# Optimization experiments

Hardware: AMD Instinct MI355X
Metric: run time of the kernel (lower is better)

## Reference

```python
import jax, jax.numpy as jnp
import numpy as np

D_MODEL = 1024
HEADS = 16
D_K = D_MODEL // HEADS
B, S = 2, 2048
NEG = -1e9


def setup_inputs() -> dict:
    key = jax.random.key(0)
    ks = jax.random.split(key, 12)
    sc = 1.0 / np.sqrt(D_MODEL)
    inp = {
        'query': jax.random.normal(ks[0], (B, S, D_MODEL), jnp.float32),
        'key': jax.random.normal(ks[1], (B, S, D_MODEL), jnp.float32),
        'value': jax.random.normal(ks[2], (B, S, D_MODEL), jnp.float32),
        'mask': jnp.tril(jnp.ones((S, S), jnp.int32))[None, None],  # [1,1,S,S] causal
        'Wq': jax.random.normal(ks[3], (D_MODEL, D_MODEL), jnp.float32) * sc,
        'bq': jax.random.normal(ks[4], (D_MODEL,), jnp.float32) * 0.02,
        'Wk': jax.random.normal(ks[5], (D_MODEL, D_MODEL), jnp.float32) * sc,
        'bk': jax.random.normal(ks[6], (D_MODEL,), jnp.float32) * 0.02,
        'Wv': jax.random.normal(ks[7], (D_MODEL, D_MODEL), jnp.float32) * sc,
        'bv': jax.random.normal(ks[8], (D_MODEL,), jnp.float32) * 0.02,
        'Wo': jax.random.normal(ks[9], (D_MODEL, D_MODEL), jnp.float32) * sc,
        'bo': jax.random.normal(ks[10], (D_MODEL,), jnp.float32) * 0.02,
    }
    return inp


def reference(query, key, value, mask, Wq, bq, Wk, bk, Wv, bv, Wo, bo):
    # QKV projections (torch Linear: x @ W.T + b; here W stored as [in,out])
    def split_heads(x):  # [B,S,D] -> [B,H,S,dk]
        return x.reshape(B, S, HEADS, D_K).transpose(0, 2, 1, 3)

    q = split_heads(query @ Wq + bq)
    k = split_heads(key @ Wk + bk)
    v = split_heads(value @ Wv + bv)

    scores = jnp.einsum('bhqd,bhkd->bhqk', q, k) / np.sqrt(D_K)
    scores = jnp.where(mask == 0, NEG, scores)
    attn = jax.nn.softmax(scores, axis=-1)  # dropout p=0 (eval) -> identity
    out = jnp.einsum('bhqk,bhkd->bhqd', attn, v)
    out = out.transpose(0, 2, 1, 3).reshape(B, S, D_MODEL)
    return out @ Wo + bo
```

## Files before the change

### kernel.cpp

```cpp
#include <hip/hip_runtime.h>
#include <hip/hip_bf16.h>
#include <cstdint>
#include <cstddef>

typedef short short8 __attribute__((ext_vector_type(8)));
typedef float f32x4 __attribute__((ext_vector_type(4)));

#define SS 2048
#define DK 64
#define LAMBDA 0.18033688011112042f

__device__ __forceinline__ float b2f(ushort u) {
    union { uint32_t i; float f; } x; x.i = ((uint32_t)u) << 16; return x.f;
}
__device__ __forceinline__ ushort f2b(float f) {
    union { float f; uint32_t i; } x; x.f = f;
    uint32_t r = (x.i + 0x7fffu + ((x.i >> 16) & 1u)) >> 16;
    return (ushort)r;
}
__device__ __forceinline__ uint32_t pk_bf16(float a, float b) {
    union { __hip_bfloat162 v; uint32_t u; } x;
    float2 f2; f2.x = a; f2.y = b;
    x.v = __float22bfloat162_rn(f2);
    return x.u;
}

__device__ __forceinline__ void gl_lds16(const ushort* __restrict__ g, ushort* l) {
    __builtin_amdgcn_global_load_lds(
        (const __attribute__((address_space(1))) uint32_t*)(uintptr_t)g,
        (__attribute__((address_space(3))) uint32_t*)(uintptr_t)l, 16, 0, 0);
}

__device__ __forceinline__ bool probe_bf16(const uint32_t* __restrict__ probe) {
    const int lane = threadIdx.x & 63;
    int c = 0;
#pragma unroll
    for (int i = 0; i < 4; ++i) {
        uint32_t u = probe[lane * 4 + i];
        uint32_t e = (u >> 7) & 0xffu;
        c += (e >= 100u && e <= 140u) ? 1 : 0;
    }
    unsigned long long b = __ballot(c >= 3);
    return __popcll(b) > 32;
}

__device__ __forceinline__ void ld8_f32_to_bf16(ushort* dst, const float* __restrict__ src) {
    float4 a = *(const float4*)src;
    float4 b = *(const float4*)(src + 4);
    ushort t[8] = {f2b(a.x), f2b(a.y), f2b(a.z), f2b(a.w),
                   f2b(b.x), f2b(b.y), f2b(b.z), f2b(b.w)};
    *(uint4*)dst = *(uint4*)t;
}

__global__ __launch_bounds__(256) void transpose_all(const void* __restrict__ W0,
                                                     const void* __restrict__ W1,
                                                     const void* __restrict__ W2,
                                                     const void* __restrict__ W3,
                                                     ushort* __restrict__ ws,
                                                     const uint32_t* __restrict__ probe,
                                                     size_t wotOff) {
    __shared__ __align__(16) ushort t[64 * 72];
    const bool isbf = probe_bf16(probe);
    const int z = blockIdx.z;
    const void* W = (z == 0) ? W0 : (z == 1) ? W1 : (z == 2) ? W2 : W3;
    ushort* T = ws + ((z < 3) ? ((size_t)z << 20) : wotOff);

    const int n0 = blockIdx.x * 64, k0 = blockIdx.y * 64;
    const int tid = threadIdx.x;
    const int r = tid >> 3, cg = (tid & 7) * 8;
    if (isbf) {
        const ushort* Wb = (const ushort*)W;
#pragma unroll
        for (int p = 0; p < 2; ++p) {
            int k = r + p * 32;
            *(uint4*)&t[k * 72 + cg] = *(const uint4*)&Wb[(size_t)(k0 + k) * 1024 + n0 + cg];
        }
    } else {
        const float* Wf = (const float*)W;
#pragma unroll
        for (int p = 0; p < 2; ++p) {
            int k = r + p * 32;
            ld8_f32_to_bf16(&t[k * 72 + cg], &Wf[(size_t)(k0 + k) * 1024 + n0 + cg]);
        }
    }
    __syncthreads();
#pragma unroll
    for (int p = 0; p < 2; ++p) {
        int n = r + p * 32;
        uint4 o;
        ushort* op = (ushort*)&o;
#pragma unroll
        for (int i = 0; i < 8; ++i) op[i] = t[(cg + i) * 72 + n];
        *(uint4*)&T[(size_t)(n0 + n) * 1024 + k0 + cg] = o;
    }
}

__global__ __launch_bounds__(256) void conv_qkv(const void* __restrict__ q,
                                                const void* __restrict__ k,
                                                const void* __restrict__ v,
                                                ushort* __restrict__ ws,
                                                const uint32_t* __restrict__ probe,
                                                size_t dstOff) {
    const bool isbf = probe_bf16(probe);
    const int z = blockIdx.y;
    const void* src = (z == 0) ? q : (z == 1) ? k : v;
    ushort* dst = ws + dstOff + ((size_t)z << 22);
    const size_t i = ((size_t)blockIdx.x * 256 + threadIdx.x) * 8;
    if (isbf)
        *(uint4*)&dst[i] = *(const uint4*)&((const ushort*)src)[i];
    else
        ld8_f32_to_bf16(&dst[i], &((const float*)src)[i]);
}

template <int PRE>
__global__ __launch_bounds__(256) void qkv_gemm(const void* __restrict__ qp,
                                                const void* __restrict__ kp,
                                                const void* __restrict__ vp,
                                                const void* __restrict__ bqp,
                                                const void* __restrict__ bkp,
                                                const void* __restrict__ bvp,
                                                ushort* __restrict__ ws,
                                                const uint32_t* __restrict__ probe) {
    __shared__ __align__(16) ushort As[128 * 32];
    __shared__ __align__(16) ushort Bs[128 * 32];
    const bool isbf = probe_bf16(probe);
    const int z = blockIdx.z;
    const ushort* Bt = ws + ((size_t)z << 20);
    const void* bias = (z == 0) ? bqp : (z == 1) ? bkp : bvp;
    ushort* C = ws + ((size_t)((PRE ? 16 : 5) + 4 * z) << 20);
    const float scl = (z == 0) ? LAMBDA : 1.0f;

    const int tid = threadIdx.x;
    const int lane = tid & 63, wid = tid >> 6;
    const int l15 = lane & 15, g = lane >> 4;
    const int wm = wid >> 1, wn = wid & 1;
    const int m0 = blockIdx.y * 128, n0 = blockIdx.x * 128;
    const int sr = tid >> 2, sc = (tid & 3) * 8;
    const int lrow = (lane >> 2), lcol = (lane & 3) * 8;

    f32x4 acc[4][4];
#pragma unroll
    for (int i = 0; i < 4; ++i)
#pragma unroll
        for (int j = 0; j < 4; ++j) {
            f32x4 zz = {0.f, 0.f, 0.f, 0.f};
            acc[i][j] = zz;
        }

    for (int kk = 0; kk < 1024; kk += 32) {
        __syncthreads();
#pragma unroll
        for (int q = 0; q < 2; ++q) {
            const int row = (wid * 2 + q) * 16 + lrow;
            gl_lds16(&Bt[(size_t)(n0 + row) * 1024 + kk + lcol], &Bs[(wid * 2 + q) * 512]);
        }
        if (PRE) {
            const ushort* Ab = ws + ((size_t)(4 + 4 * z) << 20);
#pragma unroll
            for (int q = 0; q < 2; ++q) {
                const int row = (wid * 2 + q) * 16 + lrow;
                gl_lds16(&Ab[(size_t)(m0 + row) * 1024 + kk + lcol], &As[(wid * 2 + q) * 512]);
            }
        } else {
            const void* A = (z == 0) ? qp : (z == 1) ? kp : vp;
            if (isbf) {
                const ushort* Ab = (const ushort*)A;
#pragma unroll
                for (int q = 0; q < 2; ++q) {
                    const int row = (wid * 2 + q) * 16 + lrow;
                    gl_lds16(&Ab[(size_t)(m0 + row) * 1024 + kk + lcol], &As[(wid * 2 + q) * 512]);
                }
            } else {
                const float* Af = (const float*)A;
                ld8_f32_to_bf16(&As[sr * 32 + sc], &Af[(size_t)(m0 + sr) * 1024 + kk + sc]);
                ld8_f32_to_bf16(&As[(sr + 64) * 32 + sc],
                                &Af[(size_t)(m0 + sr + 64) * 1024 + kk + sc]);
            }
        }
        __syncthreads();
        short8 a[4], b[4];
#pragma unroll
        for (int i = 0; i < 4; ++i) a[i] = *(const short8*)&As[(wm * 64 + i * 16 + l15) * 32 + g * 8];
#pragma unroll
        for (int j = 0; j < 4; ++j) b[j] = *(const short8*)&Bs[(wn * 64 + j * 16 + l15) * 32 + g * 8];
#pragma unroll
        for (int i = 0; i < 4; ++i)
#pragma unroll
            for (int j = 0; j < 4; ++j)
                acc[i][j] = __builtin_amdgcn_mfma_f32_16x16x32_bf16(a[i], b[j], acc[i][j], 0, 0, 0);
    }

#pragma unroll
    for (int i = 0; i < 4; ++i)
#pragma unroll
        for (int j = 0; j < 4; ++j) {
            const int col = n0 + wn * 64 + j * 16 + l15;
            const float bv = isbf ? b2f(((const ushort*)bias)[col]) : ((const float*)bias)[col];
#pragma unroll
            for (int r = 0; r < 4; ++r) {
                const int row = m0 + wm * 64 + i * 16 + g * 4 + r;
                const float v = (acc[i][j][r] + bv) * scl;
                size_t idx;
                if (z != 2) {
                    idx = ((size_t)((row >> 11) * 16 + (col >> 6)) * SS + (row & 2047)) * 64 +
                          (col & 63);
                } else {
                    idx = ((size_t)((row >> 11) * 16 + (col >> 6)) * 64 + (col & 63)) * SS +
                          (row & 2047);
                }
                C[idx] = f2b(v);
            }
        }
}

__global__ __launch_bounds__(256) void out_gemm(const ushort* __restrict__ A,
                                                const ushort* __restrict__ Bt,
                                                const void* __restrict__ bias,
                                                void* __restrict__ C,
                                                const uint32_t* __restrict__ probe) {
    __shared__ __align__(16) ushort As[64 * 32];
    __shared__ __align__(16) ushort Bs[128 * 32];
    const bool isbf = probe_bf16(probe);
    const int tid = threadIdx.x;
    const int lane = tid & 63, wid = tid >> 6;
    const int l15 = lane & 15, g = lane >> 4;
    const int wm = wid >> 1, wn = wid & 1;
    const int m0 = blockIdx.y * 64, n0 = blockIdx.x * 128;
    const int lrow = (lane >> 2), lcol = (lane & 3) * 8;

    f32x4 acc[2][4];
#pragma unroll
    for (int i = 0; i < 2; ++i)
#pragma unroll
        for (int j = 0; j < 4; ++j) {
            f32x4 zz = {0.f, 0.f, 0.f, 0.f};
            acc[i][j] = zz;
        }

    for (int kk = 0; kk < 1024; kk += 32) {
        __syncthreads();
        {
            const int row = wid * 16 + lrow;
            gl_lds16(&A[(size_t)(m0 + row) * 1024 + kk + lcol], &As[wid * 512]);
        }
#pragma unroll
        for (int q = 0; q < 2; ++q) {
            const int row = (wid * 2 + q) * 16 + lrow;
            gl_lds16(&Bt[(size_t)(n0 + row) * 1024 + kk + lcol], &Bs[(wid * 2 + q) * 512]);
        }
        __syncthreads();
        short8 a[2], b[4];
#pragma unroll
        for (int i = 0; i < 2; ++i) a[i] = *(const short8*)&As[(wm * 32 + i * 16 + l15) * 32 + g * 8];
#pragma unroll
        for (int j = 0; j < 4; ++j) b[j] = *(const short8*)&Bs[(wn * 64 + j * 16 + l15) * 32 + g * 8];
#pragma unroll
        for (int i = 0; i < 2; ++i)
#pragma unroll
            for (int j = 0; j < 4; ++j)
                acc[i][j] = __builtin_amdgcn_mfma_f32_16x16x32_bf16(a[i], b[j], acc[i][j], 0, 0, 0);
    }

#pragma unroll
    for (int i = 0; i < 2; ++i)
#pragma unroll
        for (int j = 0; j < 4; ++j) {
            const int col = n0 + wn * 64 + j * 16 + l15;
            const float bv = isbf ? b2f(((const ushort*)bias)[col]) : ((const float*)bias)[col];
#pragma unroll
            for (int r = 0; r < 4; ++r) {
                const int row = m0 + wm * 32 + i * 16 + g * 4 + r;
                const float v = acc[i][j][r] + bv;
                const size_t idx = (size_t)row * 1024 + col;
                if (isbf)
                    ((ushort*)C)[idx] = f2b(v);
                else
                    ((float*)C)[idx] = v;
            }
        }
}

__global__ __launch_bounds__(256, 3) void attn_fwd(const ushort* __restrict__ Q,
                                                   const ushort* __restrict__ K,
                                                   const ushort* __restrict__ Vt,
                                                   ushort* __restrict__ O) {
    __shared__ __align__(16) ushort Ks[2][64 * 64];
    __shared__ __align__(16) ushort Vs[2][64 * 64];
    __shared__ __align__(16) ushort Ps[4][32 * 64];

    const int y = blockIdx.y;
    const int s0i = (blockIdx.x + y) & 15;
    const int t = (y & 16) ? (15 - s0i) : s0i;
    const int tid = threadIdx.x;
    const int lane = tid & 63, wid = tid >> 6;
    const int l15 = lane & 15, g = lane >> 4;
    const int sw = l15 & 7;

    const ushort* Qb = Q + (size_t)y * SS * DK;
    const ushort* Kb = K + (size_t)y * SS * DK;
    const ushort* Vb = Vt + (size_t)y * DK * SS;
    const int b = y >> 4, h = y & 15;

    const int q0 = t * 128 + wid * 32;
    const int nkt = 2 * t + 2;

    const int srow = lane >> 3;
    const int sgc = ((lane & 7) ^ srow) * 8;
    ushort* Pw = Ps[wid];

    short8 qf[2][2];
#pragma unroll
    for (int mt = 0; mt < 2; ++mt)
#pragma unroll
        for (int c = 0; c < 2; ++c)
            qf[mt][c] =
                *(const short8*)&Qb[(size_t)(q0 + mt * 16 + l15) * 64 + c * 32 + g * 8];

    f32x4 acc_o[2][4];
#pragma unroll
    for (int mt = 0; mt < 2; ++mt)
#pragma unroll
        for (int jt = 0; jt < 4; ++jt) {
            f32x4 zz = {0.f, 0.f, 0.f, 0.f};
            acc_o[mt][jt] = zz;
        }
    float lp[2][4];
#pragma unroll
    for (int mt = 0; mt < 2; ++mt)
#pragma unroll
        for (int r = 0; r < 4; ++r) lp[mt][r] = 0.f;

#pragma unroll
    for (int i = 0; i < 2; ++i) {
        const int chunk = wid * 2 + i;
        const int row = chunk * 8 + srow;
        gl_lds16(&Kb[(size_t)row * 64 + sgc], &Ks[0][chunk * 512]);
        gl_lds16(&Vb[(size_t)row * SS + sgc], &Vs[0][chunk * 512]);
    }
    __syncthreads();

#pragma unroll 1
    for (int kt = 0; kt < nkt; ++kt) {
        const int cur = kt & 1;
        if (kt + 1 < nkt) {
            const int k0n = (kt + 1) * 64;
#pragma unroll
            for (int i = 0; i < 2; ++i) {
                const int chunk = wid * 2 + i;
                const int row = chunk * 8 + srow;
                gl_lds16(&Kb[(size_t)(k0n + row) * 64 + sgc], &Ks[cur ^ 1][chunk * 512]);
                gl_lds16(&Vb[(size_t)row * SS + k0n + sgc], &Vs[cur ^ 1][chunk * 512]);
            }
        }

        f32x4 sc[2][4];
#pragma unroll
        for (int mt = 0; mt < 2; ++mt)
#pragma unroll
            for (int nt = 0; nt < 4; ++nt) {
                f32x4 zz = {0.f, 0.f, 0.f, 0.f};
                sc[mt][nt] = zz;
            }
#pragma unroll
        for (int c = 0; c < 2; ++c)
#pragma unroll
            for (int nt = 0; nt < 4; ++nt) {
                short8 kb =
                    *(const short8*)&Ks[cur][(nt * 16 + l15) * 64 + (((c * 4 + g) ^ sw) * 8)];
#pragma unroll
                for (int mt = 0; mt < 2; ++mt)
                    sc[mt][nt] =
                        __builtin_amdgcn_mfma_f32_16x16x32_bf16(qf[mt][c], kb, sc[mt][nt], 0, 0, 0);
            }

        if (kt >= nkt - 2) {
            const int k0 = kt * 64;
#pragma unroll
            for (int mt = 0; mt < 2; ++mt) {
                const int rowg = q0 + mt * 16 + g * 4;
#pragma unroll
                for (int nt = 0; nt < 4; ++nt) {
                    const int colg = k0 + nt * 16 + l15;
#pragma unroll
                    for (int r = 0; r < 4; ++r)
                        if (colg > rowg + r) sc[mt][nt][r] = -1e9f;
                }
            }
        }

#pragma unroll
        for (int mt = 0; mt < 2; ++mt)
#pragma unroll
            for (int r = 0; r < 4; ++r) {
                float ss = 0.f;
#pragma unroll
                for (int nt = 0; nt < 4; ++nt) {
                    const float p = exp2f(sc[mt][nt][r]);
                    sc[mt][nt][r] = p;
                    ss += p;
                }
                lp[mt][r] += ss;
            }

#pragma unroll
        for (int mt = 0; mt < 2; ++mt)
#pragma unroll
            for (int r = 0; r < 4; ++r) {
                const int pr = mt * 16 + g * 4 + r;
                const int prsw = (pr & 7);
                const int h8 = l15 >> 3, lo3 = l15 & 7;
#pragma unroll
                for (int pp = 0; pp < 2; ++pp) {
                    const uint32_t u = pk_bf16(sc[mt][2 * pp][r], sc[mt][2 * pp + 1][r]);
                    Pw[pr * 64 + (((2 * pp) * 2 + h8) ^ prsw) * 8 + lo3] = (ushort)(u & 0xffffu);
                    Pw[pr * 64 + (((2 * pp + 1) * 2 + h8) ^ prsw) * 8 + lo3] = (ushort)(u >> 16);
                }
            }

#pragma unroll
        for (int c2 = 0; c2 < 2; ++c2) {
            short8 pa[2];
#pragma unroll
            for (int mt = 0; mt < 2; ++mt)
                pa[mt] = *(const short8*)&Pw[(mt * 16 + l15) * 64 + (((c2 * 4 + g) ^ sw) * 8)];
#pragma unroll
            for (int jt = 0; jt < 4; ++jt) {
                short8 vb =
                    *(const short8*)&Vs[cur][(jt * 16 + l15) * 64 + (((c2 * 4 + g) ^ sw) * 8)];
#pragma unroll
                for (int mt = 0; mt < 2; ++mt)
                    acc_o[mt][jt] =
                        __builtin_amdgcn_mfma_f32_16x16x32_bf16(pa[mt], vb, acc_o[mt][jt], 0, 0, 0);
            }
        }

        __syncthreads();
    }

    float inv[2][4];
#pragma unroll
    for (int mt = 0; mt < 2; ++mt)
#pragma unroll
        for (int r = 0; r < 4; ++r) {
            float ss = lp[mt][r];
            ss += __shfl_xor(ss, 1);
            ss += __shfl_xor(ss, 2);
            ss += __shfl_xor(ss, 4);
            ss += __shfl_xor(ss, 8);
            inv[mt][r] = 1.0f / ss;
        }
#pragma unroll
    for (int mt = 0; mt < 2; ++mt)
#pragma unroll
        for (int jt = 0; jt < 4; ++jt)
#pragma unroll
            for (int r = 0; r < 4; ++r) {
                const int row = q0 + mt * 16 + g * 4 + r;
                const int col = h * 64 + jt * 16 + l15;
                O[(size_t)(b * SS + row) * 1024 + col] = f2b(acc_o[mt][jt][r] * inv[mt][r]);
            }
}

extern "C" void kernel_launch(void* const* d_in, const int* in_sizes, int n_in,
                              void* d_out, int out_size, void* d_ws, size_t ws_size,
                              hipStream_t stream) {
    const void* q = d_in[0];
    const void* k = d_in[1];
    const void* v = d_in[2];
    const void* Wq = d_in[4];
    const void* bq = d_in[5];
    const void* Wk = d_in[6];
    const void* bk = d_in[7];
    const void* Wv = d_in[8];
    const void* bv = d_in[9];
    const void* Wo = d_in[10];
    const void* bo = d_in[11];
    const uint32_t* probe = (const uint32_t*)d_in[0];

    ushort* ws = (ushort*)d_ws;
    const size_t M = (size_t)1 << 20;
    const bool pre = ws_size >= 28 * M * sizeof(ushort);

    if (pre) {
        transpose_all<<<dim3(16, 16, 4), 256, 0, stream>>>(Wq, Wk, Wv, Wo, ws, probe, 3 * M);
        conv_qkv<<<dim3(2048, 3), 256, 0, stream>>>(q, k, v, ws, probe, 4 * M);
        qkv_gemm<1><<<dim3(8, 32, 3), 256, 0, stream>>>(q, k, v, bq, bk, bv, ws, probe);
        attn_fwd<<<dim3(16, 32), 256, 0, stream>>>(ws + 16 * M, ws + 20 * M, ws + 24 * M,
                                                   ws + 4 * M);
        out_gemm<<<dim3(8, 64), 256, 0, stream>>>(ws + 4 * M, ws + 3 * M, bo, d_out, probe);
    } else {
        transpose_all<<<dim3(16, 16, 4), 256, 0, stream>>>(Wq, Wk, Wv, Wo, ws, probe, 4 * M);
        qkv_gemm<0><<<dim3(8, 32, 3), 256, 0, stream>>>(q, k, v, bq, bk, bv, ws, probe);
        attn_fwd<<<dim3(16, 32), 256, 0, stream>>>(ws + 5 * M, ws + 9 * M, ws + 13 * M, ws);
        out_gemm<<<dim3(8, 64), 256, 0, stream>>>(ws, ws + 4 * M, bo, d_out, probe);
    }
}
```

Baseline: 242.8 us.

## Rewrite attention inner loop with 32x32 MFMA and register-resident P via permlane swap

```diff
diff --git a/kernel.cpp b/kernel.cpp
--- a/kernel.cpp
+++ b/kernel.cpp
@@ -5,6 +5,7 @@
 
 typedef short short8 __attribute__((ext_vector_type(8)));
 typedef float f32x4 __attribute__((ext_vector_type(4)));
+typedef float f32x16 __attribute__((ext_vector_type(16)));
 
 #define SS 2048
 #define DK 64
@@ -280,55 +281,49 @@
         }
 }
 
-__global__ __launch_bounds__(256, 3) void attn_fwd(const ushort* __restrict__ Q,
+__global__ __launch_bounds__(256, 2) void attn_fwd(const ushort* __restrict__ Q,
                                                    const ushort* __restrict__ K,
                                                    const ushort* __restrict__ Vt,
                                                    ushort* __restrict__ O) {
     __shared__ __align__(16) ushort Ks[2][64 * 64];
     __shared__ __align__(16) ushort Vs[2][64 * 64];
-    __shared__ __align__(16) ushort Ps[4][32 * 64];
 
     const int y = blockIdx.y;
     const int s0i = (blockIdx.x + y) & 15;
     const int t = (y & 16) ? (15 - s0i) : s0i;
     const int tid = threadIdx.x;
     const int lane = tid & 63, wid = tid >> 6;
-    const int l15 = lane & 15, g = lane >> 4;
-    const int sw = l15 & 7;
+    const int l31 = lane & 31, h = lane >> 5;
 
     const ushort* Qb = Q + (size_t)y * SS * DK;
     const ushort* Kb = K + (size_t)y * SS * DK;
     const ushort* Vb = Vt + (size_t)y * DK * SS;
-    const int b = y >> 4, h = y & 15;
-
-    const int q0 = t * 128 + wid * 32;
+    const int b = y >> 4, hh = y & 15;
+
+    const int q0w = t * 128 + wid * 32;
     const int nkt = 2 * t + 2;
 
     const int srow = lane >> 3;
     const int sgc = ((lane & 7) ^ srow) * 8;
-    ushort* Pw = Ps[wid];
-
-    short8 qf[2][2];
-#pragma unroll
-    for (int mt = 0; mt < 2; ++mt)
-#pragma unroll
-        for (int c = 0; c < 2; ++c)
-            qf[mt][c] =
-                *(const short8*)&Qb[(size_t)(q0 + mt * 16 + l15) * 64 + c * 32 + g * 8];
-
-    f32x4 acc_o[2][4];
-#pragma unroll
-    for (int mt = 0; mt < 2; ++mt)
-#pragma unroll
-        for (int jt = 0; jt < 4; ++jt) {
-            f32x4 zz = {0.f, 0.f, 0.f, 0.f};
-            acc_o[mt][jt] = zz;
-        }
-    float lp[2][4];
-#pragma unroll
-    for (int mt = 0; mt < 2; ++mt)
-#pragma unroll
-        for (int r = 0; r < 4; ++r) lp[mt][r] = 0.f;
+
+    short8 qf[4];
+#pragma unroll
+    for (int k4 = 0; k4 < 4; ++k4)
+        qf[k4] = *(const short8*)&Qb[(size_t)(q0w + l31) * 64 + k4 * 16 + h * 8];
+
+    int foff[2][4];
+#pragma unroll
+    for (int aa = 0; aa < 2; ++aa)
+#pragma unroll
+        for (int k4 = 0; k4 < 4; ++k4)
+            foff[aa][k4] = (aa * 32 + l31) * 64 + (((k4 * 2 + h) ^ (l31 & 7)) * 8);
+
+    f32x16 acc[2];
+#pragma unroll
+    for (int nt = 0; nt < 2; ++nt)
+#pragma unroll
+        for (int r = 0; r < 16; ++r) acc[nt][r] = 0.f;
+    float lpA = 0.f, lpB = 0.f;
 
 #pragma unroll
     for (int i = 0; i < 2; ++i) {
@@ -353,112 +348,84 @@
             }
         }
 
-        f32x4 sc[2][4];
-#pragma unroll
-        for (int mt = 0; mt < 2; ++mt)
-#pragma unroll
-            for (int nt = 0; nt < 4; ++nt) {
-                f32x4 zz = {0.f, 0.f, 0.f, 0.f};
-                sc[mt][nt] = zz;
-            }
-#pragma unroll
-        for (int c = 0; c < 2; ++c)
-#pragma unroll
-            for (int nt = 0; nt < 4; ++nt) {
-                short8 kb =
-                    *(const short8*)&Ks[cur][(nt * 16 + l15) * 64 + (((c * 4 + g) ^ sw) * 8)];
-#pragma unroll
-                for (int mt = 0; mt < 2; ++mt)
-                    sc[mt][nt] =
-                        __builtin_amdgcn_mfma_f32_16x16x32_bf16(qf[mt][c], kb, sc[mt][nt], 0, 0, 0);
-            }
-
-        if (kt >= nkt - 2) {
-            const int k0 = kt * 64;
-#pragma unroll
-            for (int mt = 0; mt < 2; ++mt) {
-                const int rowg = q0 + mt * 16 + g * 4;
-#pragma unroll
-                for (int nt = 0; nt < 4; ++nt) {
-                    const int colg = k0 + nt * 16 + l15;
-#pragma unroll
-                    for (int r = 0; r < 4; ++r)
-                        if (colg > rowg + r) sc[mt][nt][r] = -1e9f;
+        if (q0w + 31 >= kt * 64) {
+            f32x16 sc[2];
+#pragma unroll
+            for (int st = 0; st < 2; ++st)
+#pragma unroll
+                for (int r = 0; r < 16; ++r) sc[st][r] = 0.f;
+#pragma unroll
+            for (int st = 0; st < 2; ++st)
+#pragma unroll
+                for (int k4 = 0; k4 < 4; ++k4) {
+                    short8 kb = *(const short8*)&Ks[cur][foff[st][k4]];
+                    sc[st] = __builtin_amdgcn_mfma_f32_32x32x16_bf16(kb, qf[k4], sc[st], 0, 0, 0);
                 }
-            }
-        }
-
-#pragma unroll
-        for (int mt = 0; mt < 2; ++mt)
-#pragma unroll
-            for (int r = 0; r < 4; ++r) {
-                float ss = 0.f;
-#pragma unroll
-                for (int nt = 0; nt < 4; ++nt) {
-                    const float p = exp2f(sc[mt][nt][r]);
-                    sc[mt][nt][r] = p;
-                    ss += p;
+
+            if (kt >= nkt - 2) {
+                const int qg = q0w + l31;
+#pragma unroll
+                for (int st = 0; st < 2; ++st)
+#pragma unroll
+                    for (int r = 0; r < 16; ++r) {
+                        const int kvg = kt * 64 + st * 32 + (r & 3) + 8 * (r >> 2) + 4 * h;
+                        if (kvg > qg) sc[st][r] = -1e9f;
+                    }
+            }
+
+            uint32_t pk8[2][8];
+#pragma unroll
+            for (int st = 0; st < 2; ++st) {
+                float ls = 0.f;
+#pragma unroll
+                for (int i = 0; i < 8; ++i) {
+                    const float p0 = exp2f(sc[st][2 * i]);
+                    const float p1 = exp2f(sc[st][2 * i + 1]);
+                    ls += p0 + p1;
+                    pk8[st][i] = pk_bf16(p0, p1);
                 }
-                lp[mt][r] += ss;
-            }
-
-#pragma unroll
-        for (int mt = 0; mt < 2; ++mt)
-#pragma unroll
-            for (int r = 0; r < 4; ++r) {
-                const int pr = mt * 16 + g * 4 + r;
-                const int prsw = (pr & 7);
-                const int h8 = l15 >> 3, lo3 = l15 & 7;
-#pragma unroll
-                for (int pp = 0; pp < 2; ++pp) {
-                    const uint32_t u = pk_bf16(sc[mt][2 * pp][r], sc[mt][2 * pp + 1][r]);
-                    Pw[pr * 64 + (((2 * pp) * 2 + h8) ^ prsw) * 8 + lo3] = (ushort)(u & 0xffffu);
-                    Pw[pr * 64 + (((2 * pp + 1) * 2 + h8) ^ prsw) * 8 + lo3] = (ushort)(u >> 16);
+                if (st == 0) lpA += ls; else lpB += ls;
+            }
+
+#pragma unroll
+            for (int st = 0; st < 2; ++st) {
+                asm("v_permlane32_swap_b32 %0, %1" : "+v"(pk8[st][0]), "+v"(pk8[st][2]));
+                asm("v_permlane32_swap_b32 %0, %1" : "+v"(pk8[st][1]), "+v"(pk8[st][3]));
+                asm("v_permlane32_swap_b32 %0, %1" : "+v"(pk8[st][4]), "+v"(pk8[st][6]));
+                asm("v_permlane32_swap_b32 %0, %1" : "+v"(pk8[st][5]), "+v"(pk8[st][7]));
+            }
+
+#pragma unroll
+            for (int ktv = 0; ktv < 4; ++ktv) {
+                union { uint32_t u[4]; short8 s; } pa;
+#pragma unroll
+                for (int w4 = 0; w4 < 4; ++w4) pa.u[w4] = pk8[ktv >> 1][(ktv & 1) * 4 + w4];
+#pragma unroll
+                for (int nt = 0; nt < 2; ++nt) {
+                    short8 vb = *(const short8*)&Vs[cur][foff[nt][ktv]];
+                    acc[nt] =
+                        __builtin_amdgcn_mfma_f32_32x32x16_bf16(pa.s, vb, acc[nt], 0, 0, 0);
                 }
             }
-
-#pragma unroll
-        for (int c2 = 0; c2 < 2; ++c2) {
-            short8 pa[2];
-#pragma unroll
-            for (int mt = 0; mt < 2; ++mt)
-                pa[mt] = *(const short8*)&Pw[(mt * 16 + l15) * 64 + (((c2 * 4 + g) ^ sw) * 8)];
-#pragma unroll
-            for (int jt = 0; jt < 4; ++jt) {
-                short8 vb =
-                    *(const short8*)&Vs[cur][(jt * 16 + l15) * 64 + (((c2 * 4 + g) ^ sw) * 8)];
-#pragma unroll
-                for (int mt = 0; mt < 2; ++mt)
-                    acc_o[mt][jt] =
-                        __builtin_amdgcn_mfma_f32_16x16x32_bf16(pa[mt], vb, acc_o[mt][jt], 0, 0, 0);
-            }
         }
 
         __syncthreads();
     }
 
-    float inv[2][4];
-#pragma unroll
-    for (int mt = 0; mt < 2; ++mt)
-#pragma unroll
-        for (int r = 0; r < 4; ++r) {
-            float ss = lp[mt][r];
-            ss += __shfl_xor(ss, 1);
-            ss += __shfl_xor(ss, 2);
-            ss += __shfl_xor(ss, 4);
-            ss += __shfl_xor(ss, 8);
-            inv[mt][r] = 1.0f / ss;
-        }
-#pragma unroll
-    for (int mt = 0; mt < 2; ++mt)
-#pragma unroll
-        for (int jt = 0; jt < 4; ++jt)
-#pragma unroll
-            for (int r = 0; r < 4; ++r) {
-                const int row = q0 + mt * 16 + g * 4 + r;
-                const int col = h * 64 + jt * 16 + l15;
-                O[(size_t)(b * SS + row) * 1024 + col] = f2b(acc_o[mt][jt][r] * inv[mt][r]);
-            }
+    const float lp = lpA + lpB;
+    const float lt = lp + __shfl_xor(lp, 32);
+    const float inv = 1.0f / lt;
+#pragma unroll
+    for (int r = 0; r < 16; ++r) {
+        const int qrow = (r & 3) + 8 * (r >> 2) + 4 * h;
+        const float ivr = __shfl(inv, qrow);
+        const int rowg = q0w + qrow;
+#pragma unroll
+        for (int nt = 0; nt < 2; ++nt) {
+            const int col = hh * 64 + nt * 32 + l31;
+            O[(size_t)(b * SS + rowg) * 1024 + col] = f2b(acc[nt][r] * ivr);
+        }
+    }
 }
 
 extern "C" void kernel_launch(void* const* d_in, const int* in_sizes, int n_in,
```

Result: faster. 237.8 us (-2.0%).
